# Kernel tuning notes

Hardware: AMD Instinct MI355X
Metric: run time of the kernel (lower is better)

## Reference

```python
import jax, jax.numpy as jnp
import numpy as np

N_NODES = 100000
N_EDGES = 3200000
F_IN = 256
D_OUT = 64
BATCH = 4096
N_FIELDS = 20


def setup_inputs() -> dict:
    key = jax.random.key(0)
    k1, k2, k3, k4 = jax.random.split(key, 4)
    features = jax.random.normal(k1, (N_NODES, F_IN), dtype=jnp.float32)
    edge_index = jax.random.randint(k2, (2, N_EDGES), 0, N_NODES, dtype=jnp.int32)
    W = jax.random.normal(k3, (F_IN, D_OUT), dtype=jnp.float32) * 0.05
    b = jnp.zeros((D_OUT,), dtype=jnp.float32)
    x = jax.random.randint(k4, (BATCH, N_FIELDS), 0, N_NODES, dtype=jnp.int32)
    return {"features": features, "edge_index": edge_index, "W": W, "b": b, "x": x}


def reference(features, edge_index, W, b, x):
    # PyG GCNConv: add self-loops, symmetric normalization, linear transform,
    # scatter-add aggregation, then final index by x.
    n = features.shape[0]
    loop = jnp.arange(n, dtype=edge_index.dtype)
    src = jnp.concatenate([edge_index[0], loop])  # [E+N]
    dst = jnp.concatenate([edge_index[1], loop])
    ones = jnp.ones(src.shape[0], dtype=features.dtype)
    deg = jax.ops.segment_sum(ones, dst, num_segments=n)  # in-degree incl. self-loop
    deg_inv_sqrt = jnp.where(deg > 0, jax.lax.rsqrt(deg), 0.0)
    norm = deg_inv_sqrt[src] * deg_inv_sqrt[dst]  # [E+N]
    xw = features @ W  # [N, D] -- transform before aggregation (fewer FLOPs)
    msg = xw[src] * norm[:, None]  # gather + scale
    out = jax.ops.segment_sum(msg, dst, num_segments=n) + b  # [N, D]
    return out[x]  # [batch, num_fields, D]
```

## Files before the change

kernel.cpp:

```cpp
#include <hip/hip_runtime.h>
#include <hip/hip_bf16.h>

#define N_NODES 100000
#define N_EDGES 3200000
#define F_IN 256
#define D_OUT 64
#define BATCH 4096
#define N_FIELDS 20
#define N_ENTRIES (BATCH * N_FIELDS)

#define NBUCKET 512
#define NPB 196
#define N_PAD (NBUCKET * NPB)
#define EPB 4096
#define NBLK ((N_EDGES + EPB - 1) / EPB)
#define BUCKET_CAP 8192
#define CNT_BLKS (N_ENTRIES / 256)
#define GEMM_BLKS ((N_NODES + 63) / 64)
#define BCAST_BLKS (N_ENTRIES / 16)

typedef short bf16x8 __attribute__((ext_vector_type(8)));
typedef float f32x4 __attribute__((ext_vector_type(4)));

static __device__ __forceinline__ unsigned short f2bf_bits(float x) {
    __hip_bfloat16 h = __float2bfloat16(x);
    return *reinterpret_cast<unsigned short*>(&h);
}

__global__ __launch_bounds__(256) void k_front(const uint4* __restrict__ src4,
                                               const uint4* __restrict__ dst4,
                                               unsigned* __restrict__ gCursor,
                                               unsigned* __restrict__ bucketData,
                                               const int* __restrict__ x,
                                               unsigned* __restrict__ refBits,
                                               const float* __restrict__ feat,
                                               const float* __restrict__ W,
                                               float* __restrict__ yf) {
    __shared__ unsigned cur[NBUCKET];
    __shared__ unsigned short wt[64 * 264];
    int tid = threadIdx.x;

    if (blockIdx.x < NBLK) {
        cur[tid] = 0;
        cur[tid + 256] = 0;
        __syncthreads();
        int base4 = blockIdx.x * (EPB / 4);
#pragma unroll
        for (int k = 0; k < EPB / 1024; k++) {
            int e4 = base4 + k * 256 + tid;
            if (e4 < N_EDGES / 4) {
                uint4 d = dst4[e4];
                atomicAdd(&cur[d.x / NPB], 1u);
                atomicAdd(&cur[d.y / NPB], 1u);
                atomicAdd(&cur[d.z / NPB], 1u);
                atomicAdd(&cur[d.w / NPB], 1u);
            }
        }
        __syncthreads();
        unsigned c0 = cur[tid], c1 = cur[tid + 256];
        unsigned b0 = c0 ? atomicAdd(&gCursor[tid], c0) : 0u;
        unsigned b1 = c1 ? atomicAdd(&gCursor[tid + 256], c1) : 0u;
        __syncthreads();
        cur[tid] = (unsigned)tid * BUCKET_CAP + b0;
        cur[tid + 256] = (unsigned)(tid + 256) * BUCKET_CAP + b1;
        __syncthreads();
#pragma unroll
        for (int k = 0; k < EPB / 1024; k++) {
            int e4 = base4 + k * 256 + tid;
            if (e4 < N_EDGES / 4) {
                uint4 s = src4[e4];
                uint4 d = dst4[e4];
                unsigned ss[4] = {s.x, s.y, s.z, s.w};
                unsigned dd[4] = {d.x, d.y, d.z, d.w};
#pragma unroll
                for (int j = 0; j < 4; j++) {
                    unsigned b = dd[j] / NPB;
                    unsigned ld = dd[j] - b * NPB;
                    unsigned slot = atomicAdd(&cur[b], 1u);
                    if (slot < (b + 1u) * BUCKET_CAP)
                        bucketData[slot] = ss[j] | (ld << 17);
                }
            }
        }
    } else if (blockIdx.x < NBLK + CNT_BLKS) {
        int ent = (blockIdx.x - NBLK) * 256 + tid;
        if (ent < N_ENTRIES) {
            int node = x[ent];
            atomicOr(&refBits[node >> 5], 1u << (node & 31));
        }
    } else {
        int gb = blockIdx.x - NBLK - CNT_BLKS;
        {
            const float4* wrow = (const float4*)(W + tid * 64);
#pragma unroll
            for (int n4 = 0; n4 < 16; n4++) {
                float4 v = wrow[n4];
                wt[(n4 * 4 + 0) * 264 + tid] = f2bf_bits(v.x);
                wt[(n4 * 4 + 1) * 264 + tid] = f2bf_bits(v.y);
                wt[(n4 * 4 + 2) * 264 + tid] = f2bf_bits(v.z);
                wt[(n4 * 4 + 3) * 264 + tid] = f2bf_bits(v.w);
            }
        }
        __syncthreads();

        int wave = tid >> 6, lane = tid & 63;
        int quad = lane >> 4, m = lane & 15;
        int rowT = gb * 64 + wave * 16;
        int row = rowT + m;
        int rowC = (row < N_NODES) ? row : (N_NODES - 1);
        const float* fb = feat + (size_t)rowC * F_IN + quad * 8;

        f32x4 acc0 = {0.f, 0.f, 0.f, 0.f};
        f32x4 acc1 = acc0, acc2 = acc0, acc3 = acc0;

#pragma unroll
        for (int kk = 0; kk < 8; kk++) {
            float4 x0 = *(const float4*)(fb + kk * 32);
            float4 x1 = *(const float4*)(fb + kk * 32 + 4);
            bf16x8 a;
            a[0] = (short)f2bf_bits(x0.x); a[1] = (short)f2bf_bits(x0.y);
            a[2] = (short)f2bf_bits(x0.z); a[3] = (short)f2bf_bits(x0.w);
            a[4] = (short)f2bf_bits(x1.x); a[5] = (short)f2bf_bits(x1.y);
            a[6] = (short)f2bf_bits(x1.z); a[7] = (short)f2bf_bits(x1.w);
            int kbase = kk * 32 + quad * 8;
            bf16x8 b0 = *(const bf16x8*)&wt[(0 * 16 + m) * 264 + kbase];
            bf16x8 b1 = *(const bf16x8*)&wt[(1 * 16 + m) * 264 + kbase];
            bf16x8 b2 = *(const bf16x8*)&wt[(2 * 16 + m) * 264 + kbase];
            bf16x8 b3 = *(const bf16x8*)&wt[(3 * 16 + m) * 264 + kbase];
            acc0 = __builtin_amdgcn_mfma_f32_16x16x32_bf16(a, b0, acc0, 0, 0, 0);
            acc1 = __builtin_amdgcn_mfma_f32_16x16x32_bf16(a, b1, acc1, 0, 0, 0);
            acc2 = __builtin_amdgcn_mfma_f32_16x16x32_bf16(a, b2, acc2, 0, 0, 0);
            acc3 = __builtin_amdgcn_mfma_f32_16x16x32_bf16(a, b3, acc3, 0, 0, 0);
        }

#pragma unroll
        for (int r = 0; r < 4; r++) {
            int rr = rowT + quad * 4 + r;
            if (rr < N_NODES) {
                size_t o = (size_t)rr * D_OUT + m;
                yf[o]      = acc0[r];
                yf[o + 16] = acc1[r];
                yf[o + 32] = acc2[r];
                yf[o + 48] = acc3[r];
            }
        }
    }
}

__global__ __launch_bounds__(256) void k_bucket_csr(unsigned* __restrict__ bucketData,
                                                    const unsigned* __restrict__ gCursor,
                                                    const unsigned* __restrict__ refBits,
                                                    int* __restrict__ rowStart,
                                                    unsigned short* __restrict__ deg,
                                                    const float* __restrict__ yf,
                                                    unsigned short* __restrict__ y) {
    __shared__ unsigned srcsorted[BUCKET_CAP];
    __shared__ unsigned nodeCount[NPB];
    __shared__ unsigned sscan[256];
    __shared__ unsigned cursor[NPB];
    __shared__ unsigned char refF[NPB];

    int b = blockIdx.x;
    int base = b * BUCKET_CAP;
    int cnt = (int)gCursor[b];
    if (cnt > BUCKET_CAP) cnt = BUCKET_CAP;
    int tid = threadIdx.x;

    for (int j = tid; j < NPB; j += 256) nodeCount[j] = 0;
    __syncthreads();

    for (int i = tid; i < cnt; i += 256) {
        unsigned w = bucketData[base + i];
        atomicAdd(&nodeCount[w >> 17], 1u);
    }
    __syncthreads();

    int firstNode = b * NPB;
    unsigned refCnt = 0;
    if (tid < NPB) {
        int node = firstNode + tid;
        unsigned isRef = (refBits[node >> 5] >> (node & 31)) & 1u;
        refF[tid] = (unsigned char)isRef;
        refCnt = isRef ? nodeCount[tid] : 0;
        deg[node] = (unsigned short)nodeCount[tid];
    }
    sscan[tid] = refCnt;
    __syncthreads();
    for (int off = 1; off < 256; off <<= 1) {
        unsigned t = (tid >= off) ? sscan[tid - off] : 0;
        __syncthreads();
        sscan[tid] += t;
        __syncthreads();
    }

    if (tid < NPB) {
        unsigned excl = sscan[tid] - refCnt;
        rowStart[firstNode + tid] = base + (int)excl;
        cursor[tid] = excl;
    }
    __syncthreads();

    for (int i = tid; i < cnt; i += 256) {
        unsigned w = bucketData[base + i];
        unsigned ld = w >> 17;
        if (refF[ld]) {
            unsigned slot = atomicAdd(&cursor[ld], 1u);
            srcsorted[slot] = w & 0x1FFFFu;
        }
    }
    __syncthreads();

    int refTotal = (int)sscan[255];
    for (int i = tid; i < refTotal; i += 256)
        bucketData[base + i] = srcsorted[i];

    for (int idx = tid; idx < NPB * 16; idx += 256) {
        int j = idx >> 4;
        int node = firstNode + j;
        if (node < N_NODES) {
            float ds = rsqrtf((float)nodeCount[j] + 1.0f);
            float4 v = ((const float4*)(yf + (size_t)node * D_OUT))[idx & 15];
            uint2 pw;
            pw.x = (unsigned)f2bf_bits(v.x * ds) | ((unsigned)f2bf_bits(v.y * ds) << 16);
            pw.y = (unsigned)f2bf_bits(v.z * ds) | ((unsigned)f2bf_bits(v.w * ds) << 16);
            ((uint2*)(y + (size_t)node * D_OUT))[idx & 15] = pw;
        }
    }
}

static __device__ __forceinline__ void acc4(f32x4& a, uint2 v, float msk) {
    a[0] += msk * __uint_as_float(v.x << 16);
    a[1] += msk * __uint_as_float(v.x & 0xffff0000u);
    a[2] += msk * __uint_as_float(v.y << 16);
    a[3] += msk * __uint_as_float(v.y & 0xffff0000u);
}

__global__ __launch_bounds__(256) void k_agg(const unsigned* __restrict__ refBits,
                                             const int* __restrict__ rowStart,
                                             const unsigned short* __restrict__ deg,
                                             const unsigned* __restrict__ sortedSrc,
                                             const unsigned short* __restrict__ y,
                                             const float* __restrict__ b,
                                             float* __restrict__ valN) {
    int g = blockIdx.x * blockDim.x + threadIdx.x;
    int i = g >> 6, lane = g & 63;
    if (i >= N_PAD) return;
    if (!((refBits[i >> 5] >> (i & 31)) & 1u)) return;

    int grp = lane >> 4;
    int m = lane & 15;
    int start = rowStart[i];
    int cnt = deg[i];
    float disI = rsqrtf((float)(cnt + 1));

    uint2 sv = *(const uint2*)(y + ((unsigned)i << 6) + (m << 2));

    f32x4 a0 = {0.f, 0.f, 0.f, 0.f};
    f32x4 a1 = a0, a2 = a0, a3 = a0;

    for (int e = 0; e < cnt; e += 32) {
        int e0 = e + grp,      e1 = e + 4 + grp,  e2 = e + 8 + grp,  e3 = e + 12 + grp;
        int e4 = e + 16 + grp, e5 = e + 20 + grp, e6 = e + 24 + grp, e7 = e + 28 + grp;
        unsigned r0 = (e0 < cnt) ? sortedSrc[start + e0] : (unsigned)i;
        unsigned r1 = (e1 < cnt) ? sortedSrc[start + e1] : (unsigned)i;
        unsigned r2 = (e2 < cnt) ? sortedSrc[start + e2] : (unsigned)i;
        unsigned r3 = (e3 < cnt) ? sortedSrc[start + e3] : (unsigned)i;
        unsigned r4 = (e4 < cnt) ? sortedSrc[start + e4] : (unsigned)i;
        unsigned r5 = (e5 < cnt) ? sortedSrc[start + e5] : (unsigned)i;
        unsigned r6 = (e6 < cnt) ? sortedSrc[start + e6] : (unsigned)i;
        unsigned r7 = (e7 < cnt) ? sortedSrc[start + e7] : (unsigned)i;
        uint2 v0 = *(const uint2*)(y + (r0 << 6) + (m << 2));
        uint2 v1 = *(const uint2*)(y + (r1 << 6) + (m << 2));
        uint2 v2 = *(const uint2*)(y + (r2 << 6) + (m << 2));
        uint2 v3 = *(const uint2*)(y + (r3 << 6) + (m << 2));
        uint2 v4 = *(const uint2*)(y + (r4 << 6) + (m << 2));
        uint2 v5 = *(const uint2*)(y + (r5 << 6) + (m << 2));
        uint2 v6 = *(const uint2*)(y + (r6 << 6) + (m << 2));
        uint2 v7 = *(const uint2*)(y + (r7 << 6) + (m << 2));
        acc4(a0, v0, (e0 < cnt) ? 1.f : 0.f);
        acc4(a1, v1, (e1 < cnt) ? 1.f : 0.f);
        acc4(a2, v2, (e2 < cnt) ? 1.f : 0.f);
        acc4(a3, v3, (e3 < cnt) ? 1.f : 0.f);
        acc4(a0, v4, (e4 < cnt) ? 1.f : 0.f);
        acc4(a1, v5, (e5 < cnt) ? 1.f : 0.f);
        acc4(a2, v6, (e6 < cnt) ? 1.f : 0.f);
        acc4(a3, v7, (e7 < cnt) ? 1.f : 0.f);
    }

    f32x4 s;
#pragma unroll
    for (int c = 0; c < 4; c++) s[c] = (a0[c] + a1[c]) + (a2[c] + a3[c]);
#pragma unroll
    for (int c = 0; c < 4; c++) {
        s[c] += __shfl_xor(s[c], 16, 64);
        s[c] += __shfl_xor(s[c], 32, 64);
    }

    if (grp == 0) {
        float4 b4 = *(const float4*)(b + (m << 2));
        float4 val;
        val.x = disI * (s[0] + __uint_as_float(sv.x << 16)) + b4.x;
        val.y = disI * (s[1] + __uint_as_float(sv.x & 0xffff0000u)) + b4.y;
        val.z = disI * (s[2] + __uint_as_float(sv.y << 16)) + b4.z;
        val.w = disI * (s[3] + __uint_as_float(sv.y & 0xffff0000u)) + b4.w;
        *(float4*)(valN + (size_t)i * D_OUT + (m << 2)) = val;
    }
}

__global__ __launch_bounds__(256) void k_bcast(const int* __restrict__ x,
                                               const float* __restrict__ valN,
                                               float* __restrict__ out) {
    int tid = threadIdx.x;
    int ent = blockIdx.x * 16 + (tid >> 4);
    int q = tid & 15;
    int node = x[ent];
    float4 v = ((const float4*)(valN + (size_t)node * D_OUT))[q];
    ((float4*)(out + (size_t)ent * D_OUT))[q] = v;
}

extern "C" void kernel_launch(void* const* d_in, const int* in_sizes, int n_in,
                              void* d_out, int out_size, void* d_ws, size_t ws_size,
                              hipStream_t stream) {
    const float* feat     = (const float*)d_in[0];
    const int* edge_index = (const int*)d_in[1];
    const float* W        = (const float*)d_in[2];
    const float* bsrc     = (const float*)d_in[3];
    const int* x          = (const int*)d_in[4];
    float* out            = (float*)d_out;

    const uint4* src4 = (const uint4*)edge_index;
    const uint4* dst4 = (const uint4*)(edge_index + N_EDGES);

    char* ws = (char*)d_ws;
    size_t off = 0;
    auto alloc = [&](size_t bytes) {
        size_t o = off;
        off = (off + bytes + 255) & ~(size_t)255;
        return o;
    };
    unsigned* gCursor   = (unsigned*)(ws + alloc((size_t)NBUCKET * 4));
    unsigned* refBits   = (unsigned*)(ws + alloc((size_t)(N_PAD / 8)));
    int* rowStart       = (int*)(ws + alloc((size_t)N_PAD * 4));
    unsigned short* deg = (unsigned short*)(ws + alloc((size_t)N_PAD * 2));
    unsigned* bucketData = (unsigned*)(ws + alloc((size_t)NBUCKET * BUCKET_CAP * 4));
    unsigned short* y   = (unsigned short*)(ws + alloc((size_t)N_NODES * D_OUT * 2));
    float* yf           = (float*)(ws + alloc((size_t)N_NODES * D_OUT * 4));
    float* valN         = (float*)(ws + alloc((size_t)N_PAD * D_OUT * 4));
    (void)ws_size; (void)in_sizes; (void)n_in; (void)out_size;

    const int T = 256;
    (void)hipMemsetAsync(gCursor, 0, (size_t)NBUCKET * 4, stream);
    (void)hipMemsetAsync(refBits, 0, (size_t)(N_PAD / 8), stream);
    k_front<<<NBLK + CNT_BLKS + GEMM_BLKS, T, 0, stream>>>(src4, dst4, gCursor, bucketData,
                                                           x, refBits, feat, W, yf);
    k_bucket_csr<<<NBUCKET, T, 0, stream>>>(bucketData, gCursor, refBits, rowStart, deg, yf, y);
    k_agg<<<((size_t)N_PAD * 64 + T - 1) / T, T, 0, stream>>>(
        refBits, rowStart, deg, bucketData, y, bsrc, valN);
    k_bcast<<<BCAST_BLKS, T, 0, stream>>>(x, valN, out);
}
```

Baseline: 319.8 us.

## Locally sort edges by bucket in shared memory before coalesced global scatter

Each edge-binning block now handles twice as many edges and first scatters them into a shared-memory sort buffer ordered by bucket, using a block-wide prefix scan over bucket counts. It then writes the sorted buffer to global bucket storage contiguously, finding each element's bucket by binary search. The goal is to turn scattered single-word global writes into mostly contiguous runs and to cut the number of global cursor atomics. The cost is extra shared memory, scan and search work, and more barriers.

```diff
diff --git a/kernel.cpp b/kernel.cpp
--- a/kernel.cpp
+++ b/kernel.cpp
@@ -12,12 +12,17 @@
 #define NBUCKET 512
 #define NPB 196
 #define N_PAD (NBUCKET * NPB)
-#define EPB 4096
+#define EPB 8192
 #define NBLK ((N_EDGES + EPB - 1) / EPB)
 #define BUCKET_CAP 8192
 #define CNT_BLKS (N_ENTRIES / 256)
 #define GEMM_BLKS ((N_NODES + 63) / 64)
 #define BCAST_BLKS (N_ENTRIES / 16)
+
+#define SB_BYTES   (EPB * 4)
+#define LBE_OFF    SB_BYTES
+#define CUR_OFF    (LBE_OFF + 2052)
+#define SBG_OFF    (CUR_OFF + 2048)
 
 typedef short bf16x8 __attribute__((ext_vector_type(8)));
 typedef float f32x4 __attribute__((ext_vector_type(4)));
@@ -36,11 +41,15 @@
                                                const float* __restrict__ feat,
                                                const float* __restrict__ W,
                                                float* __restrict__ yf) {
-    __shared__ unsigned cur[NBUCKET];
-    __shared__ unsigned short wt[64 * 264];
+    __shared__ __align__(16) char smem[38928];
     int tid = threadIdx.x;
 
     if (blockIdx.x < NBLK) {
+        unsigned* sortbuf = (unsigned*)smem;
+        int*      lbE     = (int*)(smem + LBE_OFF);
+        unsigned* cur     = (unsigned*)(smem + CUR_OFF);
+        unsigned* sbG     = (unsigned*)(smem + SBG_OFF);
+
         cur[tid] = 0;
         cur[tid + 256] = 0;
         __syncthreads();
@@ -58,11 +67,28 @@
         }
         __syncthreads();
         unsigned c0 = cur[tid], c1 = cur[tid + 256];
-        unsigned b0 = c0 ? atomicAdd(&gCursor[tid], c0) : 0u;
-        unsigned b1 = c1 ? atomicAdd(&gCursor[tid + 256], c1) : 0u;
-        __syncthreads();
-        cur[tid] = (unsigned)tid * BUCKET_CAP + b0;
-        cur[tid + 256] = (unsigned)(tid + 256) * BUCKET_CAP + b1;
+        unsigned g0 = c0 ? atomicAdd(&gCursor[tid], c0) : 0u;
+        unsigned g1 = c1 ? atomicAdd(&gCursor[tid + 256], c1) : 0u;
+        sbG[tid] = (unsigned)tid * BUCKET_CAP + g0;
+        sbG[tid + 256] = (unsigned)(tid + 256) * BUCKET_CAP + g1;
+        lbE[tid] = (int)c0;
+        lbE[tid + 256] = (int)c1;
+        __syncthreads();
+        for (int off = 1; off < 512; off <<= 1) {
+            int t0 = (tid >= off) ? lbE[tid - off] : 0;
+            int t1 = lbE[tid + 256 - off];
+            __syncthreads();
+            lbE[tid] += t0;
+            lbE[tid + 256] += t1;
+            __syncthreads();
+        }
+        int incl0 = lbE[tid], incl1 = lbE[tid + 256];
+        __syncthreads();
+        lbE[tid] = incl0 - (int)c0;
+        lbE[tid + 256] = incl1 - (int)c1;
+        cur[tid] = (unsigned)(incl0 - (int)c0);
+        cur[tid + 256] = (unsigned)(incl1 - (int)c1);
+        if (tid == 255) lbE[NBUCKET] = incl1;
         __syncthreads();
 #pragma unroll
         for (int k = 0; k < EPB / 1024; k++) {
@@ -77,10 +103,22 @@
                     unsigned b = dd[j] / NPB;
                     unsigned ld = dd[j] - b * NPB;
                     unsigned slot = atomicAdd(&cur[b], 1u);
-                    if (slot < (b + 1u) * BUCKET_CAP)
-                        bucketData[slot] = ss[j] | (ld << 17);
+                    sortbuf[slot] = ss[j] | (ld << 17);
                 }
             }
+        }
+        __syncthreads();
+        int ecnt = lbE[NBUCKET];
+        for (int i = tid; i < ecnt; i += 256) {
+            unsigned w = sortbuf[i];
+            int lo = 0, hi = NBUCKET;
+            while (hi - lo > 1) {
+                int mid = (lo + hi) >> 1;
+                if (lbE[mid] <= i) lo = mid; else hi = mid;
+            }
+            unsigned dstIdx = sbG[lo] + (unsigned)(i - lbE[lo]);
+            if (dstIdx < (unsigned)(lo + 1) * BUCKET_CAP)
+                bucketData[dstIdx] = w;
         }
     } else if (blockIdx.x < NBLK + CNT_BLKS) {
         int ent = (blockIdx.x - NBLK) * 256 + tid;
@@ -89,6 +127,7 @@
             atomicOr(&refBits[node >> 5], 1u << (node & 31));
         }
     } else {
+        unsigned short* wt = (unsigned short*)smem;
         int gb = blockIdx.x - NBLK - CNT_BLKS;
         {
             const float4* wrow = (const float4*)(W + tid * 64);
```

Result: faster. 285.4 us (-10.8%).
